# Optimization experiments

Hardware: AMD Instinct MI355X
Metric: run time of the kernel (lower is better)

## Reference

```python
import jax, jax.numpy as jnp
import numpy as np

N = 10000        # num nodes
E = 640000       # num edges
FIN = 128        # input feature dim
NH = 8           # num heads
FOUT = 16        # out features per head (NH*FOUT == FIN)
NEG_SLOPE = 0.2
EPS = 1e-16


def setup_inputs() -> dict:
    key = jax.random.key(0)
    ks = jax.random.split(key, 7)
    x = jax.random.normal(ks[0], (N, FIN), dtype=jnp.float32)
    edges = jax.random.randint(ks[1], (2, E), 0, N, dtype=jnp.int64)
    # kaiming-uniform-ish init scale
    s = float(np.sqrt(6.0 / FIN))
    W_proj = jax.random.uniform(ks[2], (NH * FOUT, FIN), minval=-s, maxval=s, dtype=jnp.float32)
    W_skip = jax.random.uniform(ks[3], (NH * FOUT, FIN), minval=-s, maxval=s, dtype=jnp.float32)
    sf = float(np.sqrt(6.0 / FOUT))
    score_src = jax.random.uniform(ks[4], (1, NH, FOUT), minval=-sf, maxval=sf, dtype=jnp.float32)
    score_tgt = jax.random.uniform(ks[5], (1, NH, FOUT), minval=-sf, maxval=sf, dtype=jnp.float32)
    bias = jnp.zeros((NH * FOUT,), dtype=jnp.float32)
    return {"x": x, "edges": edges, "W_proj": W_proj, "W_skip": W_skip,
            "score_src": score_src, "score_tgt": score_tgt, "bias": bias}


def reference(x, edges, W_proj, W_skip, score_src, score_tgt, bias):
    src, tgt = edges[0], edges[1]
    # project: [N, NH, FOUT]
    proj = (x @ W_proj.T).reshape(N, NH, FOUT)
    # per-node scores: [N, NH]
    s_src = (proj * score_src).sum(-1)
    s_tgt = (proj * score_tgt).sum(-1)
    # lift to edges and score: [E, NH]
    scores = jax.nn.leaky_relu(s_src[src] + s_tgt[tgt], negative_slope=NEG_SLOPE)
    # neighborhood-aware softmax (global max subtraction, as in original)
    exp_scores = jnp.exp(scores - jnp.max(scores))
    denom = jax.ops.segment_sum(exp_scores, tgt, num_segments=N)  # [N, NH]
    att = exp_scores / (denom[tgt] + EPS)                          # [E, NH]
    # weighted aggregation: [N, NH, FOUT]
    weighted = proj[src] * att[:, :, None]
    out = jax.ops.segment_sum(weighted, tgt, num_segments=N)
    # skip connection (dims differ per-head, so skip_proj is used), concat, bias
    out = out + (x @ W_skip.T).reshape(N, NH, FOUT)
    out = out.reshape(N, NH * FOUT) + bias
    return out
```

## Files before the change

kernel.cpp:

```cpp
#include <hip/hip_runtime.h>
#include <hip/hip_bf16.h>

#define FIN   128
#define NH    8
#define NEG   0.2f
#define HB    128
#define NMAX  10240

typedef __attribute__((ext_vector_type(8))) short short8;
typedef __attribute__((ext_vector_type(4))) float f32x4;

__device__ __forceinline__ short f2bf(float f) {
    unsigned u = __float_as_uint(f);
    return (short)((u + 0x7FFFu + ((u >> 16) & 1u)) >> 16);
}
__device__ __forceinline__ float bflo(unsigned p) { return __uint_as_float(p << 16); }
__device__ __forceinline__ float bfhi(unsigned p) { return __uint_as_float(p & 0xFFFF0000u); }
__device__ __forceinline__ float ld_f(const void* p, int i, bool bf16) {
    if (bf16) {
        unsigned h = ((const unsigned short*)p)[i];
        return __uint_as_float(h << 16);
    }
    return ((const float*)p)[i];
}
__device__ __forceinline__ short8 ld_frag(const void* p, size_t off, bool bf16) {
    if (bf16) return *(const short8*)((const short*)p + off);
    const float* f = (const float*)p + off;
    f32x4 f0 = *(const f32x4*)f;
    f32x4 f1 = *(const f32x4*)(f + 4);
    short8 r;
    r[0] = f2bf(f0[0]); r[1] = f2bf(f0[1]); r[2] = f2bf(f0[2]); r[3] = f2bf(f0[3]);
    r[4] = f2bf(f1[0]); r[5] = f2bf(f1[1]); r[6] = f2bf(f1[2]); r[7] = f2bf(f1[3]);
    return r;
}
__device__ __forceinline__ float escore(float ss, float st) {
    float v = ss + st;
    v = v > 0.f ? v : NEG * v;
    return __expf(fminf(v, 60.f));
}
__device__ __forceinline__ bool wave_bf16(const unsigned* x32) {
    unsigned w  = x32[threadIdx.x & 63];
    unsigned ex = (w >> 7) & 0xFFu;
    return __popcll(__ballot(ex >= 118u && ex <= 130u)) >= 48;
}
__device__ __forceinline__ bool wave_e64(const int* e32) {
    return __popcll(__ballot(e32[2 * (threadIdx.x & 63) + 1] == 0)) == 64;
}

__global__ __launch_bounds__(256) void k_projhist(
    const void* __restrict__ x, const void* __restrict__ Wp,
    const void* __restrict__ Ws,
    const void* __restrict__ ssrcw, const void* __restrict__ stgtw,
    unsigned short* __restrict__ projb, unsigned short* __restrict__ skipb,
    float* __restrict__ s_src, float* __restrict__ s_tgt,
    const int* __restrict__ e32, int* __restrict__ hist2d,
    int N, int E, int tiles, int halfTiles, int projBlocks, int perB)
{
    __shared__ unsigned l32[NMAX / 2];
    if ((int)blockIdx.x >= projBlocks) {
        const bool e64 = wave_e64(e32);
        const int hb = (int)blockIdx.x - projBlocks;
        const int t = threadIdx.x;
        const int nw = (N + 1) >> 1;
        for (int j = t; j < nw; j += 256) l32[j] = 0;
        __syncthreads();
        const int lo = hb * perB;
        const int hi = min(lo + perB, E);
        for (int i = lo + t; i < hi; i += 256) {
            int tg = e64 ? e32[2 * ((size_t)E + i)] : e32[(size_t)E + i];
            atomicAdd(&l32[tg >> 1], 1u << ((tg & 1) << 4));
        }
        __syncthreads();
        for (int j = t; j < N; j += 256)
            hist2d[(size_t)hb * N + j] = (l32[j >> 1] >> ((j & 1) << 4)) & 0xFFFFu;
        return;
    }
    const bool bf16 = wave_bf16((const unsigned*)x);
    const int lane = threadIdx.x & 63;
    const int wt = blockIdx.x * 4 + (threadIdx.x >> 6);
    if (wt >= tiles) return;
    const int mat = (wt >= halfTiles) ? 1 : 0;
    const int m0 = (mat ? wt - halfTiles : wt) * 16;
    const int mr = lane & 15;
    const int kb = lane >> 4;

    short8 a[4];
    const size_t xoff = (size_t)(m0 + mr) * FIN + kb * 8;
#pragma unroll
    for (int s = 0; s < 4; ++s) a[s] = ld_frag(x, xoff + s * 32, bf16);

    const void* W = mat ? Ws : Wp;
    f32x4 acc[8];
#pragma unroll
    for (int c = 0; c < 8; ++c) {
        acc[c] = (f32x4){0.f, 0.f, 0.f, 0.f};
        const size_t woff = (size_t)(c * 16 + mr) * FIN + kb * 8;
#pragma unroll
        for (int s = 0; s < 4; ++s) {
            short8 b = ld_frag(W, woff + s * 32, bf16);
            acc[c] = __builtin_amdgcn_mfma_f32_16x16x32_bf16(a[s], b, acc[c], 0, 0, 0);
        }
    }
    if (mat == 0) {
#pragma unroll
        for (int c = 0; c < 8; ++c) {
            float sw = ld_f(ssrcw, c * 16 + mr, bf16);
            float tw = ld_f(stgtw, c * 16 + mr, bf16);
#pragma unroll
            for (int r = 0; r < 4; ++r) {
                int row = m0 + kb * 4 + r;
                float v = acc[c][r];
                projb[(size_t)row * FIN + c * 16 + mr] = (unsigned short)f2bf(v);
                float vs = v * sw, vt = v * tw;
#pragma unroll
                for (int o = 8; o >= 1; o >>= 1) {
                    vs += __shfl_xor(vs, o);
                    vt += __shfl_xor(vt, o);
                }
                if (mr == 0) {
                    s_src[row * NH + c] = vs;
                    s_tgt[row * NH + c] = vt;
                }
            }
        }
    } else {
#pragma unroll
        for (int c = 0; c < 8; ++c)
#pragma unroll
            for (int r = 0; r < 4; ++r)
                skipb[(size_t)(m0 + kb * 4 + r) * FIN + c * 16 + mr] =
                    (unsigned short)f2bf(acc[c][r]);
    }
}

__global__ __launch_bounds__(256) void k_colscan(
    const int* __restrict__ hist2d, int* __restrict__ pbase,
    int* __restrict__ cnt, int N)
{
    int j = blockIdx.x * 256 + threadIdx.x;
    if (j >= N) return;
    int s = 0;
#pragma unroll 4
    for (int b = 0; b < HB; ++b) {
        int v = hist2d[(size_t)b * N + j];
        pbase[(size_t)b * N + j] = s;
        s += v;
    }
    cnt[j] = s;
}

__global__ __launch_bounds__(256) void k_place(
    const int* __restrict__ e32, const int* __restrict__ cnt,
    const int* __restrict__ pbase, int* __restrict__ offs,
    int* __restrict__ sorted_src, int N, int E, int perB)
{
    __shared__ int cur[NMAX];
    __shared__ int sd[256];
    const bool e64 = wave_e64(e32);
    const int b = blockIdx.x, t = threadIdx.x;

    const int PER = (N + 255) / 256;
    const int base = t * PER;
    int local[40];
    int sum = 0;
    for (int i = 0; i < PER && i < 40; ++i) {
        int idx = base + i;
        int v = (idx < N) ? cnt[idx] : 0;
        local[i] = sum;
        sum += v;
    }
    sd[t] = sum;
    __syncthreads();
#pragma unroll
    for (int off = 1; off < 256; off <<= 1) {
        int add = (t >= off) ? sd[t - off] : 0;
        __syncthreads();
        sd[t] += add;
        __syncthreads();
    }
    const int excl = sd[t] - sum;
    for (int i = 0; i < PER && i < 40; ++i) {
        int idx = base + i;
        if (idx < N) {
            int o = excl + local[i];
            cur[idx] = o + pbase[(size_t)b * N + idx];
            if (b == 0) offs[idx] = o;
        }
    }
    if (b == 0 && t == 255) offs[N] = sd[255];
    __syncthreads();

    const int lo = b * perB;
    const int hi = min(lo + perB, E);
    for (int i = lo + t; i < hi; i += 256) {
        int s, tg;
        if (e64) { s = e32[2 * (size_t)i]; tg = e32[2 * ((size_t)E + i)]; }
        else     { s = e32[i];             tg = e32[(size_t)E + i]; }
        int pos = atomicAdd(&cur[tg], 1);
        sorted_src[pos] = s;
    }
}

__global__ __launch_bounds__(64) void k_aggregate(
    const int* __restrict__ offs, const int* __restrict__ sorted_src,
    const float* __restrict__ s_src, const float* __restrict__ s_tgt,
    const unsigned short* __restrict__ projb, const unsigned short* __restrict__ skipb,
    const void* __restrict__ bias, void* __restrict__ out,
    const unsigned* __restrict__ x32)
{
    const bool bf16 = wave_bf16(x32);
    const int n = blockIdx.x, l = threadIdx.x;
    const int start = offs[n], end = offs[n + 1];
    const int h = l >> 3;
    const int c2 = l * 2;
    const float st = s_tgt[(size_t)n * NH + h];

    float ae0 = 0.f, ao0 = 0.f, ae1 = 0.f, ao1 = 0.f;
    float ae2 = 0.f, ao2 = 0.f, ae3 = 0.f, ao3 = 0.f;
    float d0 = 0.f, d1 = 0.f, d2 = 0.f, d3 = 0.f;

    const int cnt4 = (end - start) >> 2;
    int e = start;
    if (cnt4 > 0) {
        int s0 = sorted_src[e],     s1 = sorted_src[e + 1];
        int s2 = sorted_src[e + 2], s3 = sorted_src[e + 3];
        for (int g = 0; g < cnt4; ++g) {
            const int t0 = s0, t1 = s1, t2 = s2, t3 = s3;
            e += 4;
            if (g + 1 < cnt4) {
                s0 = sorted_src[e];     s1 = sorted_src[e + 1];
                s2 = sorted_src[e + 2]; s3 = sorted_src[e + 3];
            }
            float w0 = escore(s_src[(size_t)t0 * NH + h], st);
            float w1 = escore(s_src[(size_t)t1 * NH + h], st);
            float w2 = escore(s_src[(size_t)t2 * NH + h], st);
            float w3 = escore(s_src[(size_t)t3 * NH + h], st);
            unsigned p0 = *(const unsigned*)(projb + (size_t)t0 * FIN + c2);
            unsigned p1 = *(const unsigned*)(projb + (size_t)t1 * FIN + c2);
            unsigned p2 = *(const unsigned*)(projb + (size_t)t2 * FIN + c2);
            unsigned p3 = *(const unsigned*)(projb + (size_t)t3 * FIN + c2);
            ae0 += w0 * bflo(p0); ao0 += w0 * bfhi(p0); d0 += w0;
            ae1 += w1 * bflo(p1); ao1 += w1 * bfhi(p1); d1 += w1;
            ae2 += w2 * bflo(p2); ao2 += w2 * bfhi(p2); d2 += w2;
            ae3 += w3 * bflo(p3); ao3 += w3 * bfhi(p3); d3 += w3;
        }
    }
    for (; e < end; ++e) {
        int s = sorted_src[e];
        float w = escore(s_src[(size_t)s * NH + h], st);
        unsigned p = *(const unsigned*)(projb + (size_t)s * FIN + c2);
        ae0 += w * bflo(p); ao0 += w * bfhi(p); d0 += w;
    }

    float inv = 1.f / (((d0 + d1) + (d2 + d3)) + 1e-16f);
    unsigned skp = *(const unsigned*)(skipb + (size_t)n * FIN + c2);
    float be, bo;
    if (bf16) {
        unsigned bb = *(const unsigned*)((const unsigned short*)bias + c2);
        be = bflo(bb); bo = bfhi(bb);
    } else {
        float2 b2 = *(const float2*)((const float*)bias + c2);
        be = b2.x; bo = b2.y;
    }
    float oe = ((ae0 + ae1) + (ae2 + ae3)) * inv + bflo(skp) + be;
    float oo = ((ao0 + ao1) + (ao2 + ao3)) * inv + bfhi(skp) + bo;
    if (bf16) {
        unsigned pr = ((unsigned)(unsigned short)f2bf(oo) << 16)
                    | (unsigned)(unsigned short)f2bf(oe);
        ((unsigned*)out)[((size_t)n * FIN + c2) >> 1] = pr;
    } else {
        float2 o2; o2.x = oe; o2.y = oo;
        *(float2*)((float*)out + (size_t)n * FIN + c2) = o2;
    }
}

extern "C" void kernel_launch(void* const* d_in, const int* in_sizes, int n_in,
                              void* d_out, int out_size, void* d_ws, size_t ws_size,
                              hipStream_t stream)
{
    const void* x    = d_in[0];
    const int* edges = (const int*)d_in[1];
    const void* Wp   = d_in[2];
    const void* Ws   = d_in[3];
    const void* ssw  = d_in[4];
    const void* stw  = d_in[5];
    const void* bias = d_in[6];

    const int N = in_sizes[0] / FIN;
    const int E = in_sizes[1] / 2;

    unsigned short* projb = (unsigned short*)d_ws;
    unsigned short* skipb = projb + (size_t)N * FIN;
    float* s_src    = (float*)(skipb + (size_t)N * FIN);
    float* s_tgt    = s_src + (size_t)N * NH;
    int* sorted_src = (int*)(s_tgt + (size_t)N * NH);
    int* offs       = sorted_src + E;
    int* cnt        = offs + (N + 1);
    int* hist2d     = cnt + N;
    int* pbase      = hist2d + (size_t)HB * N;

    const int halfTiles  = (N + 15) / 16;
    const int tiles      = 2 * halfTiles;
    const int projBlocks = (tiles + 3) / 4;
    const int perB       = (E + HB - 1) / HB;

    k_projhist<<<projBlocks + HB, 256, 0, stream>>>(
        x, Wp, Ws, ssw, stw, projb, skipb, s_src, s_tgt,
        edges, hist2d, N, E, tiles, halfTiles, projBlocks, perB);
    k_colscan<<<(N + 255) / 256, 256, 0, stream>>>(hist2d, pbase, cnt, N);
    k_place<<<HB, 256, 0, stream>>>(edges, cnt, pbase, offs, sorted_src, N, E, perB);
    k_aggregate<<<N, 64, 0, stream>>>(offs, sorted_src, s_src, s_tgt, projb,
                                      skipb, bias, d_out, (const unsigned*)x);
}
```

Baseline: 165.9 us.

## Double histogram blocks, vectorize place prefix scan, batch edge loads before atomics

Raises the number of histogram/placement blocks from 128 to 256 so the counting-sort phases use more CUs with fewer edges each. k_place now reads counts and per-block bases as int4 on a fast path when N is a multiple of 4 and PER is 40. It also preloads up to 10 edges per thread into registers before issuing the LDS atomics, to overlap memory latency. Workspace buffers are 256-byte aligned and cnt is padded so the vector loads stay in bounds. The cost is double the hist2d/pbase size and a longer column scan in k_colscan.

Result: faster. 148.0 us (-10.8%).

```diff
diff --git a/kernel.cpp b/kernel.cpp
--- a/kernel.cpp
+++ b/kernel.cpp
@@ -4,7 +4,7 @@
 #define FIN   128
 #define NH    8
 #define NEG   0.2f
-#define HB    128
+#define HB    256
 #define NMAX  10240
 
 typedef __attribute__((ext_vector_type(8))) short short8;
@@ -135,12 +135,12 @@
 
 __global__ __launch_bounds__(256) void k_colscan(
     const int* __restrict__ hist2d, int* __restrict__ pbase,
-    int* __restrict__ cnt, int N)
+    int* __restrict__ cnt, int N, int Npad)
 {
     int j = blockIdx.x * 256 + threadIdx.x;
-    if (j >= N) return;
+    if (j >= N) { if (j < Npad) cnt[j] = 0; return; }
     int s = 0;
-#pragma unroll 4
+#pragma unroll 8
     for (int b = 0; b < HB; ++b) {
         int v = hist2d[(size_t)b * N + j];
         pbase[(size_t)b * N + j] = s;
@@ -158,41 +158,98 @@
     __shared__ int sd[256];
     const bool e64 = wave_e64(e32);
     const int b = blockIdx.x, t = threadIdx.x;
-
     const int PER = (N + 255) / 256;
-    const int base = t * PER;
-    int local[40];
-    int sum = 0;
-    for (int i = 0; i < PER && i < 40; ++i) {
-        int idx = base + i;
-        int v = (idx < N) ? cnt[idx] : 0;
-        local[i] = sum;
-        sum += v;
-    }
-    sd[t] = sum;
-    __syncthreads();
-#pragma unroll
-    for (int off = 1; off < 256; off <<= 1) {
-        int add = (t >= off) ? sd[t - off] : 0;
+
+    if (PER == 40 && (N & 3) == 0) {
+        const int4* c4 = (const int4*)cnt + t * 10;
+        int4 v[10];
+        int sum = 0;
+#pragma unroll
+        for (int q = 0; q < 10; ++q) {
+            v[q] = c4[q];
+            sum += (v[q].x + v[q].y) + (v[q].z + v[q].w);
+        }
+        sd[t] = sum;
         __syncthreads();
-        sd[t] += add;
+#pragma unroll
+        for (int off = 1; off < 256; off <<= 1) {
+            int add = (t >= off) ? sd[t - off] : 0;
+            __syncthreads();
+            sd[t] += add;
+            __syncthreads();
+        }
+        int run = sd[t] - sum;
+        const int base = t * 40;
+        const int4* pb4 = (const int4*)(pbase + (size_t)b * N) + t * 10;
+#pragma unroll
+        for (int q = 0; q < 10; ++q) {
+            int4 pb = pb4[q];
+            int idx = base + q * 4;
+            int r0 = run;
+            int r1 = r0 + v[q].x;
+            int r2 = r1 + v[q].y;
+            int r3 = r2 + v[q].z;
+            cur[idx]     = r0 + pb.x;
+            cur[idx + 1] = r1 + pb.y;
+            cur[idx + 2] = r2 + pb.z;
+            cur[idx + 3] = r3 + pb.w;
+            if (b == 0) {
+                if (idx     < N) offs[idx]     = r0;
+                if (idx + 1 < N) offs[idx + 1] = r1;
+                if (idx + 2 < N) offs[idx + 2] = r2;
+                if (idx + 3 < N) offs[idx + 3] = r3;
+            }
+            run = r3 + v[q].w;
+        }
+        if (b == 0 && t == 255) offs[N] = run;
+    } else {
+        int sum = 0;
+        for (int i = 0; i < PER; ++i) {
+            int idx = t * PER + i;
+            sum += (idx < N) ? cnt[idx] : 0;
+        }
+        sd[t] = sum;
         __syncthreads();
-    }
-    const int excl = sd[t] - sum;
-    for (int i = 0; i < PER && i < 40; ++i) {
-        int idx = base + i;
-        if (idx < N) {
-            int o = excl + local[i];
-            cur[idx] = o + pbase[(size_t)b * N + idx];
-            if (b == 0) offs[idx] = o;
-        }
-    }
-    if (b == 0 && t == 255) offs[N] = sd[255];
+#pragma unroll
+        for (int off = 1; off < 256; off <<= 1) {
+            int add = (t >= off) ? sd[t - off] : 0;
+            __syncthreads();
+            sd[t] += add;
+            __syncthreads();
+        }
+        int run = sd[t] - sum;
+        for (int i = 0; i < PER; ++i) {
+            int idx = t * PER + i;
+            if (idx < N) {
+                cur[idx] = run + pbase[(size_t)b * N + idx];
+                if (b == 0) offs[idx] = run;
+                run += cnt[idx];
+            }
+        }
+        if (b == 0 && t == 255) offs[N] = run;
+    }
     __syncthreads();
 
     const int lo = b * perB;
     const int hi = min(lo + perB, E);
-    for (int i = lo + t; i < hi; i += 256) {
+    int se[10], te[10];
+#pragma unroll
+    for (int k = 0; k < 10; ++k) {
+        int i = lo + t + k * 256;
+        te[k] = -1;
+        if (i < hi) {
+            if (e64) { se[k] = e32[2 * (size_t)i]; te[k] = e32[2 * ((size_t)E + i)]; }
+            else     { se[k] = e32[i];             te[k] = e32[(size_t)E + i]; }
+        }
+    }
+#pragma unroll
+    for (int k = 0; k < 10; ++k) {
+        if (te[k] >= 0) {
+            int pos = atomicAdd(&cur[te[k]], 1);
+            sorted_src[pos] = se[k];
+        }
+    }
+    for (int i = lo + t + 10 * 256; i < hi; i += 256) {
         int s, tg;
         if (e64) { s = e32[2 * (size_t)i]; tg = e32[2 * ((size_t)E + i)]; }
         else     { s = e32[i];             tg = e32[(size_t)E + i]; }
@@ -288,16 +345,24 @@
 
     const int N = in_sizes[0] / FIN;
     const int E = in_sizes[1] / 2;
-
-    unsigned short* projb = (unsigned short*)d_ws;
-    unsigned short* skipb = projb + (size_t)N * FIN;
-    float* s_src    = (float*)(skipb + (size_t)N * FIN);
-    float* s_tgt    = s_src + (size_t)N * NH;
-    int* sorted_src = (int*)(s_tgt + (size_t)N * NH);
-    int* offs       = sorted_src + E;
-    int* cnt        = offs + (N + 1);
-    int* hist2d     = cnt + N;
-    int* pbase      = hist2d + (size_t)HB * N;
+    const int PER  = (N + 255) / 256;
+    const int Npad = PER * 256;
+
+    char* wp = (char*)d_ws;
+    auto takeB = [&wp](size_t bytes) {
+        char* p = wp;
+        wp += (bytes + 255) & ~(size_t)255;
+        return p;
+    };
+    unsigned short* projb = (unsigned short*)takeB((size_t)N * FIN * 2);
+    unsigned short* skipb = (unsigned short*)takeB((size_t)N * FIN * 2);
+    float* s_src    = (float*)takeB((size_t)N * NH * 4);
+    float* s_tgt    = (float*)takeB((size_t)N * NH * 4);
+    int* sorted_src = (int*)takeB((size_t)E * 4);
+    int* offs       = (int*)takeB((size_t)(N + 8) * 4);
+    int* cnt        = (int*)takeB((size_t)Npad * 4);
+    int* hist2d     = (int*)takeB((size_t)HB * N * 4);
+    int* pbase      = (int*)takeB((size_t)HB * N * 4 + 4096);
 
     const int halfTiles  = (N + 15) / 16;
     const int tiles      = 2 * halfTiles;
@@ -307,7 +372,7 @@
     k_projhist<<<projBlocks + HB, 256, 0, stream>>>(
         x, Wp, Ws, ssw, stw, projb, skipb, s_src, s_tgt,
         edges, hist2d, N, E, tiles, halfTiles, projBlocks, perB);
-    k_colscan<<<(N + 255) / 256, 256, 0, stream>>>(hist2d, pbase, cnt, N);
+    k_colscan<<<Npad / 256, 256, 0, stream>>>(hist2d, pbase, cnt, N, Npad);
     k_place<<<HB, 256, 0, stream>>>(edges, cnt, pbase, offs, sorted_src, N, E, perB);
     k_aggregate<<<N, 64, 0, stream>>>(offs, sorted_src, s_src, s_tgt, projb,
                                       skipb, bias, d_out, (const unsigned*)x);
```
